# Kernel tuning notes

Hardware: AMD Instinct MI355X
Metric: run time of the kernel (lower is better)

## Reference

```python
import jax, jax.numpy as jnp
import numpy as np

D_MODEL = 1024
NUM_HEADS = 16
D_K = D_MODEL // NUM_HEADS
NEG_INF = -1e9


def setup_inputs() -> dict:
    key = jax.random.key(0)
    ks = jax.random.split(key, 12)
    B, S = 2, 2048
    Q = jax.random.normal(ks[0], (B, S, D_MODEL), jnp.float32)
    K = jax.random.normal(ks[1], (B, S, D_MODEL), jnp.float32)
    V = jax.random.normal(ks[2], (B, S, D_MODEL), jnp.float32)
    mask = jax.random.randint(ks[3], (B, 1, 1, S), 0, 2, jnp.int32)
    scale = 1.0 / np.sqrt(D_MODEL)
    WQ = jax.random.normal(ks[4], (D_MODEL, D_MODEL), jnp.float32) * scale
    bQ = jnp.zeros((D_MODEL,), jnp.float32)
    WK = jax.random.normal(ks[5], (D_MODEL, D_MODEL), jnp.float32) * scale
    bK = jnp.zeros((D_MODEL,), jnp.float32)
    WV = jax.random.normal(ks[6], (D_MODEL, D_MODEL), jnp.float32) * scale
    bV = jnp.zeros((D_MODEL,), jnp.float32)
    WO = jax.random.normal(ks[7], (D_MODEL, D_MODEL), jnp.float32) * scale
    bO = jnp.zeros((D_MODEL,), jnp.float32)
    return {"Q": Q, "K": K, "V": V, "mask": mask,
            "WQ": WQ, "bQ": bQ, "WK": WK, "bK": bK,
            "WV": WV, "bV": bV, "WO": WO, "bO": bO}


def _split_heads(x):
    # (B, S, d_model) -> (B, H, S, d_k)
    B, S, _ = x.shape
    return x.reshape(B, S, NUM_HEADS, D_K).transpose(0, 2, 1, 3)


def reference(Q, K, V, mask, WQ, bQ, WK, bK, WV, bV, WO, bO):
    B, Sq, _ = Q.shape
    q = _split_heads(Q @ WQ + bQ)   # (B, H, Sq, d_k)
    k = _split_heads(K @ WK + bK)   # (B, H, Sk, d_k)
    v = _split_heads(V @ WV + bV)   # (B, H, Sk, d_v)
    scores = jnp.einsum('bhqd,bhkd->bhqk', q, k) / jnp.sqrt(jnp.float32(D_K))
    scores = jnp.where(mask == 0, jnp.float32(NEG_INF), scores)
    attention = jax.nn.softmax(scores, axis=-1)         # (B, H, Sq, Sk)
    context = jnp.einsum('bhqk,bhkd->bhqd', attention, v)
    context = context.transpose(0, 2, 1, 3).reshape(B, Sq, D_MODEL)
    output = context @ WO + bO
    return (output, attention)
```

## Files before the change

### kernel.cpp

```cpp
#include <hip/hip_runtime.h>

typedef __attribute__((ext_vector_type(8))) __bf16 bf16x8;
typedef __attribute__((ext_vector_type(4))) __bf16 bf16x4;
typedef __attribute__((ext_vector_type(4))) float f32x4;

#define DEVFN static __device__ __forceinline__

#if __has_builtin(__builtin_amdgcn_exp2f)
#define EXP2(x) __builtin_amdgcn_exp2f(x)
#else
#define EXP2(x) exp2f(x)
#endif

DEVFN f32x4 mfma16(bf16x8 a, bf16x8 b, f32x4 c) {
  return __builtin_amdgcn_mfma_f32_16x16x32_bf16(a, b, c, 0, 0, 0);
}

DEVFN void gload16(const void* g, void* l) {
  __builtin_amdgcn_global_load_lds((const __attribute__((address_space(1))) void*)g,
                                   (__attribute__((address_space(3))) void*)l, 16, 0, 0);
}

__global__ __launch_bounds__(256) void transW4(const float* __restrict__ w0,
                                               const float* __restrict__ w1,
                                               const float* __restrict__ w2,
                                               const float* __restrict__ w3,
                                               unsigned short* __restrict__ obase) {
  __shared__ float t[64][65];
  const float* W = blockIdx.z == 0 ? w0 : blockIdx.z == 1 ? w1 : blockIdx.z == 2 ? w2 : w3;
  unsigned short* Wt = obase + ((size_t)blockIdx.z << 20);
  int k0 = blockIdx.x * 64, n0 = blockIdx.y * 64;
  int tid = threadIdx.x;
#pragma unroll
  for (int it = 0; it < 4; ++it) {
    int r = it * 16 + (tid >> 4);
    int c = (tid & 15) * 4;
    float4 v = *(const float4*)(W + (size_t)(k0 + r) * 1024 + n0 + c);
    t[r][c] = v.x; t[r][c + 1] = v.y; t[r][c + 2] = v.z; t[r][c + 3] = v.w;
  }
  __syncthreads();
#pragma unroll
  for (int it = 0; it < 2; ++it) {
    int nl = it * 32 + (tid >> 3);
    int kc = tid & 7;
    bf16x8 o;
#pragma unroll
    for (int j = 0; j < 8; ++j) o[j] = (__bf16)t[kc * 8 + j][nl];
    int n = n0 + nl;
    char* dst = (char*)Wt + (size_t)n * 2048 + (k0 << 1) + ((kc ^ (n & 7)) << 4);
    *(bf16x8*)dst = o;
  }
}

struct GArg {
  const void* A;
  const unsigned short* Bt;
  const float* bias;
  void* out;
  float scale;
};

template <int BM, int BN, int WR, int WC, int AF32, int EPI>
__global__ __launch_bounds__(256, 2) void gemm_t(GArg g0, GArg g1, GArg g2) {
  GArg g = blockIdx.z == 0 ? g0 : blockIdx.z == 1 ? g1 : g2;
  constexpr int MT = BM / WR / 16, NT = BN / WC / 16;
  constexpr int AB = AF32 ? 4 : 2;
  __shared__ char lA[BM * 64 * AB];
  __shared__ char lB[BN * 64 * 2];
  int tid = threadIdx.x, wave = tid >> 6, lane = tid & 63;
  int hi = lane >> 4, lo = lane & 15;
  int m0 = blockIdx.x * BM, n0 = blockIdx.y * BN;
  int wr = wave / WC, wc = wave % WC;
  f32x4 acc[MT][NT];
#pragma unroll
  for (int mt = 0; mt < MT; ++mt)
#pragma unroll
    for (int nt = 0; nt < NT; ++nt) acc[mt][nt] = (f32x4){0.f, 0.f, 0.f, 0.f};

  for (int k0 = 0; k0 < 1024; k0 += 64) {
    if (AF32) {
#pragma unroll
      for (int i = 0; i < BM / 16; ++i) {
        int off = i * 4096 + tid * 16;
        int row = off >> 8, b = off & 255;
        gload16((const char*)g.A + (size_t)(m0 + row) * 4096 + (k0 << 2)
                    + (b ^ ((row & 7) << 4)),
                lA + i * 4096 + wave * 1024);
      }
    } else {
#pragma unroll
      for (int i = 0; i < BM / 32; ++i) {
        int off = i * 4096 + tid * 16;
        int row = off >> 7, b = off & 127;
        gload16((const char*)g.A + (size_t)(m0 + row) * 2048 + (k0 << 1) + b,
                lA + i * 4096 + wave * 1024);
      }
    }
#pragma unroll
    for (int i = 0; i < BN / 32; ++i) {
      int off = i * 4096 + tid * 16;
      int row = off >> 7, b = off & 127;
      gload16((const char*)g.Bt + (size_t)(n0 + row) * 2048 + (k0 << 1) + b,
              lB + i * 4096 + wave * 1024);
    }
    __syncthreads();
#pragma unroll
    for (int kk = 0; kk < 2; ++kk) {
      bf16x8 af[MT], bfr[NT];
#pragma unroll
      for (int mt = 0; mt < MT; ++mt) {
        int row = wr * (BM / WR) + mt * 16 + lo;
        if (AF32) {
          int base = (row << 8) + ((kk << 7) + (hi << 5));
          int sw = (row & 7) << 4;
          f32x4 a0 = *(const f32x4*)(lA + ((base) ^ sw));
          f32x4 a1 = *(const f32x4*)(lA + ((base + 16) ^ sw));
          bf16x8 v;
#pragma unroll
          for (int j = 0; j < 4; ++j) { v[j] = (__bf16)a0[j]; v[4 + j] = (__bf16)a1[j]; }
          af[mt] = v;
        } else {
          int ob = (row << 7) + ((((kk << 2) + hi) << 4) ^ ((row & 7) << 4));
          af[mt] = *(const bf16x8*)(lA + ob);
        }
      }
#pragma unroll
      for (int nt = 0; nt < NT; ++nt) {
        int row = wc * (BN / WC) + nt * 16 + lo;
        int ob = (row << 7) + ((((kk << 2) + hi) << 4) ^ ((row & 7) << 4));
        bfr[nt] = *(const bf16x8*)(lB + ob);
      }
#pragma unroll
      for (int mt = 0; mt < MT; ++mt)
#pragma unroll
        for (int nt = 0; nt < NT; ++nt)
          acc[mt][nt] = mfma16(af[mt], bfr[nt], acc[mt][nt]);
    }
    __syncthreads();
  }

#pragma unroll
  for (int mt = 0; mt < MT; ++mt) {
#pragma unroll
    for (int nt = 0; nt < NT; ++nt) {
      int col = n0 + wc * (BN / WC) + nt * 16 + lo;
      float bs = g.bias[col];
      int row0 = m0 + wr * (BM / WR) + mt * 16 + (hi << 2);
      float vj[4];
#pragma unroll
      for (int j = 0; j < 4; ++j) vj[j] = (acc[mt][nt][j] + bs) * g.scale;
      if (EPI == 1) {
#pragma unroll
        for (int j = 0; j < 4; ++j)
          ((float*)g.out)[(size_t)(row0 + j) * 1024 + col] = vj[j];
      } else if (blockIdx.z == 2) {
        int d = col & 63;
        int bh = (row0 >> 11) * 16 + (col >> 6);
        int s = row0 & 2047;
        bf16x4 o;
#pragma unroll
        for (int j = 0; j < 4; ++j) o[j] = (__bf16)vj[j];
        char* p = (char*)g.out + ((size_t)bh << 18) + (size_t)d * 4096
                  + (s >> 6) * 128 + (((((s & 63) >> 3) ^ (d & 7)) << 4))
                  + ((s & 7) << 1);
        *(bf16x4*)p = o;
      } else {
#pragma unroll
        for (int j = 0; j < 4; ++j) {
          int srow = row0 + j;
          size_t hb = ((size_t)((srow >> 11) * 16 + (col >> 6))) << 18;
          int ib = ((srow & 2047) << 7) + (((col & 63) << 1) ^ ((srow & 7) << 4));
          *(__bf16*)((char*)g.out + hb + ib) = (__bf16)vj[j];
        }
      }
    }
  }
}

__global__ __launch_bounds__(256, 4) void attn_k(
    const unsigned short* __restrict__ qh, const unsigned short* __restrict__ kh,
    const unsigned short* __restrict__ vt, const int* __restrict__ mask,
    float* __restrict__ attn, unsigned short* __restrict__ ctx) {
  constexpr int S = 2048;
  __shared__ unsigned short ktl[64 * 64];
  __shared__ unsigned short vtl[64 * 64];
  __shared__ unsigned long long mkb[32];
  __shared__ float pf[4][16 * 68];

  int tid = threadIdx.x, wave = tid >> 6, lane = tid & 63;
  int hi = lane >> 4, lo = lane & 15;
  int f = blockIdx.y * 32 + blockIdx.x;
  int xcd = f & 7, slot = f >> 3;
  int bh = xcd * 4 + (slot & 3);
  int qb = slot >> 2;
  int b = bh >> 4, h = bh & 15;
  const char* khead = (const char*)kh + ((size_t)bh << 18);
  const char* qhead = (const char*)qh + ((size_t)bh << 18);
  const char* vhead = (const char*)vt + ((size_t)bh << 18);

  for (int it = 0; it < 8; ++it) {
    unsigned long long bal = __ballot(mask[b * S + it * 256 + tid] != 0);
    if (lane == 0) mkb[it * 4 + wave] = bal;
  }
  __syncthreads();

  int q0 = qb * 64 + wave * 16;
  bf16x8 qf[2];
  {
    int row = q0 + lo;
#pragma unroll
    for (int kk = 0; kk < 2; ++kk) {
      int ib = (row << 7) + ((((kk << 2) + hi) << 4) ^ ((row & 7) << 4));
      qf[kk] = *(const bf16x8*)(qhead + ib);
    }
  }

  float lsum[4] = {0.f, 0.f, 0.f, 0.f};

#pragma unroll
  for (int i = 0; i < 2; ++i)
    gload16(khead + i * 4096 + tid * 16, (char*)ktl + i * 4096 + wave * 1024);
  for (int kt = 0; kt < 32; ++kt) {
    const char* cb = (kt & 1) ? (const char*)vtl : (const char*)ktl;
    char* nb = (kt & 1) ? (char*)ktl : (char*)vtl;
    if (kt < 31) {
#pragma unroll
      for (int i = 0; i < 2; ++i)
        gload16(khead + (size_t)(kt + 1) * 8192 + i * 4096 + tid * 16,
                nb + i * 4096 + wave * 1024);
      asm volatile("s_waitcnt vmcnt(2)" ::: "memory");
    } else {
      asm volatile("s_waitcnt vmcnt(0)" ::: "memory");
    }
    __builtin_amdgcn_sched_barrier(0);
    __builtin_amdgcn_s_barrier();
    unsigned long long mw = mkb[kt];
    __builtin_amdgcn_s_setprio(1);
#pragma unroll
    for (int nt = 0; nt < 4; ++nt) {
      int r = nt * 16 + lo;
      f32x4 a = {0.f, 0.f, 0.f, 0.f};
#pragma unroll
      for (int kk = 0; kk < 2; ++kk) {
        int ob = (r << 7) + ((((kk << 2) + hi) << 4) ^ ((r & 7) << 4));
        a = mfma16(qf[kk], *(const bf16x8*)(cb + ob), a);
      }
      bool ok = (mw >> r) & 1ull;
#pragma unroll
      for (int j = 0; j < 4; ++j) lsum[j] += ok ? EXP2(a[j]) : 0.f;
    }
    __builtin_amdgcn_s_setprio(0);
    __builtin_amdgcn_s_barrier();
  }

  float rcp[4];
#pragma unroll
  for (int j = 0; j < 4; ++j) {
    float s = lsum[j];
    s += __shfl_xor(s, 1); s += __shfl_xor(s, 2);
    s += __shfl_xor(s, 4); s += __shfl_xor(s, 8);
    rcp[j] = s > 0.f ? 1.0f / s : 0.f;
  }

  f32x4 cacc[4];
#pragma unroll
  for (int nt = 0; nt < 4; ++nt) cacc[nt] = (f32x4){0.f, 0.f, 0.f, 0.f};

  float* arow = attn + (size_t)bh * S * S;
  float* pfw = pf[wave];

  for (int kt = 0; kt < 32; ++kt) {
#pragma unroll
    for (int i = 0; i < 2; ++i)
      gload16(khead + (size_t)kt * 8192 + i * 4096 + tid * 16,
              (char*)ktl + i * 4096 + wave * 1024);
#pragma unroll
    for (int i = 0; i < 2; ++i) {
      int off = i * 4096 + tid * 16;
      int d = off >> 7, x = off & 127;
      gload16(vhead + (size_t)d * 4096 + kt * 128 + x,
              (char*)vtl + i * 4096 + wave * 1024);
    }
    __syncthreads();
    unsigned long long mw = mkb[kt];
    __builtin_amdgcn_s_setprio(1);
#pragma unroll
    for (int nt = 0; nt < 4; ++nt) {
      int r = nt * 16 + lo;
      f32x4 a = {0.f, 0.f, 0.f, 0.f};
#pragma unroll
      for (int kk = 0; kk < 2; ++kk) {
        int ob = (r << 7) + ((((kk << 2) + hi) << 4) ^ ((r & 7) << 4));
        a = mfma16(qf[kk], *(const bf16x8*)((const char*)ktl + ob), a);
      }
      bool ok = (mw >> r) & 1ull;
#pragma unroll
      for (int j = 0; j < 4; ++j) {
        float pn = ok ? EXP2(a[j]) * rcp[j] : 0.f;
        pfw[((hi << 2) + j) * 68 + r] = pn;
      }
    }
#pragma unroll
    for (int c = 0; c < 2; ++c) {
      f32x4 p0 = *(const f32x4*)&pfw[lo * 68 + c * 32 + hi * 8];
      f32x4 p1 = *(const f32x4*)&pfw[lo * 68 + c * 32 + hi * 8 + 4];
      bf16x8 pa;
#pragma unroll
      for (int i = 0; i < 4; ++i) { pa[i] = (__bf16)p0[i]; pa[4 + i] = (__bf16)p1[i]; }
#pragma unroll
      for (int nt = 0; nt < 4; ++nt) {
        int d = nt * 16 + lo;
        int ob = (d << 7) + ((((c << 2) + hi) << 4) ^ ((d & 7) << 4));
        cacc[nt] = mfma16(pa, *(const bf16x8*)((const char*)vtl + ob), cacc[nt]);
      }
    }
    __builtin_amdgcn_s_setprio(0);
    {
      int rsub = lane >> 4;
      int cb = (lane & 15) << 2;
#pragma unroll
      for (int s = 0; s < 4; ++s) {
        int row = s * 4 + rsub;
        f32x4 v = *(const f32x4*)&pfw[row * 68 + cb];
        __builtin_nontemporal_store(
            v, (f32x4*)(arow + (size_t)(q0 + row) * S + kt * 64 + cb));
      }
    }
    __syncthreads();
  }

#pragma unroll
  for (int nt = 0; nt < 4; ++nt) {
#pragma unroll
    for (int j = 0; j < 4; ++j) {
      int s = q0 + (hi << 2) + j;
      int mrow = b * S + s;
      int n = h * 64 + nt * 16 + lo;
      int ib = (n << 1) ^ ((mrow & 7) << 4);
      *(__bf16*)((char*)ctx + (size_t)mrow * 2048 + ib) = (__bf16)cacc[nt][j];
    }
  }
}

extern "C" void kernel_launch(void* const* d_in, const int* in_sizes, int n_in,
                              void* d_out, int out_size, void* d_ws, size_t ws_size,
                              hipStream_t stream) {
  const float* Q  = (const float*)d_in[0];
  const float* K  = (const float*)d_in[1];
  const float* V  = (const float*)d_in[2];
  const int* mask = (const int*)d_in[3];
  const float* WQ = (const float*)d_in[4];
  const float* bQ = (const float*)d_in[5];
  const float* WK = (const float*)d_in[6];
  const float* bK = (const float*)d_in[7];
  const float* WV = (const float*)d_in[8];
  const float* bV = (const float*)d_in[9];
  const float* WO = (const float*)d_in[10];
  const float* bO = (const float*)d_in[11];

  char* ws = (char*)d_ws;
  const size_t M1 = 1ull << 20;
  unsigned short* WQt = (unsigned short*)(ws + 0 * M1);
  unsigned short* WKt = (unsigned short*)(ws + 2 * M1);
  unsigned short* WVt = (unsigned short*)(ws + 4 * M1);
  unsigned short* WOt = (unsigned short*)(ws + 6 * M1);
  unsigned short* qh  = (unsigned short*)(ws + 8 * M1);
  unsigned short* kh  = (unsigned short*)(ws + 16 * M1);
  unsigned short* vt  = (unsigned short*)(ws + 24 * M1);
  unsigned short* ctx = (unsigned short*)(ws + 32 * M1);

  float* outF = (float*)d_out;
  float* attn = (float*)d_out + 4194304;

  dim3 blk(256);
  const float qscale = 0.125f * 1.44269504088896340736f;

  transW4<<<dim3(16, 16, 4), blk, 0, stream>>>(WQ, WK, WV, WO, WQt);

  GArg aq{Q, WQt, bQ, qh, qscale};
  GArg ak{K, WKt, bK, kh, 1.f};
  GArg av{V, WVt, bV, vt, 1.f};
  gemm_t<128, 128, 2, 2, 1, 0><<<dim3(32, 8, 3), blk, 0, stream>>>(aq, ak, av);

  attn_k<<<dim3(32, 32), blk, 0, stream>>>(qh, kh, vt, mask, attn, ctx);

  GArg ao{ctx, WOt, bO, outF, 1.f};
  gemm_t<64, 128, 1, 4, 0, 1><<<dim3(64, 8, 1), blk, 0, stream>>>(ao, ao, ao);
}
```

Baseline: 246.4 us.

## Rework attention pass-1 K loading, reorder attention stores, raise QKV GEMM occupancy

The first (row-sum) pass of the attention kernel drops its double-buffered, prefetching K loop. It now loads two 64-key tiles into both LDS buffers at once, with a full __syncthreads, and processes them as one 128-key step. This halves the number of barriers but gives up the overlap between loads and compute. In the second pass the attention-probability store to global memory moves ahead of the P·V MFMAs and becomes a normal store instead of a nontemporal one. The QKV projection GEMM gets a launch-bounds occupancy hint of 3 blocks per CU instead of 2, which may limit its registers.

```diff
diff --git a/kernel.cpp b/kernel.cpp
--- a/kernel.cpp
+++ b/kernel.cpp
@@ -60,8 +60,8 @@
   float scale;
 };
 
-template <int BM, int BN, int WR, int WC, int AF32, int EPI>
-__global__ __launch_bounds__(256, 2) void gemm_t(GArg g0, GArg g1, GArg g2) {
+template <int BM, int BN, int WR, int WC, int AF32, int EPI, int OCC>
+__global__ __launch_bounds__(256, OCC) void gemm_t(GArg g0, GArg g1, GArg g2) {
   GArg g = blockIdx.z == 0 ? g0 : blockIdx.z == 1 ? g1 : g2;
   constexpr int MT = BM / WR / 16, NT = BN / WC / 16;
   constexpr int AB = AF32 ? 4 : 2;
@@ -217,40 +217,37 @@
 
   float lsum[4] = {0.f, 0.f, 0.f, 0.f};
 
-#pragma unroll
-  for (int i = 0; i < 2; ++i)
-    gload16(khead + i * 4096 + tid * 16, (char*)ktl + i * 4096 + wave * 1024);
-  for (int kt = 0; kt < 32; ++kt) {
-    const char* cb = (kt & 1) ? (const char*)vtl : (const char*)ktl;
-    char* nb = (kt & 1) ? (char*)ktl : (char*)vtl;
-    if (kt < 31) {
-#pragma unroll
-      for (int i = 0; i < 2; ++i)
-        gload16(khead + (size_t)(kt + 1) * 8192 + i * 4096 + tid * 16,
-                nb + i * 4096 + wave * 1024);
-      asm volatile("s_waitcnt vmcnt(2)" ::: "memory");
-    } else {
-      asm volatile("s_waitcnt vmcnt(0)" ::: "memory");
-    }
-    __builtin_amdgcn_sched_barrier(0);
-    __builtin_amdgcn_s_barrier();
-    unsigned long long mw = mkb[kt];
+  for (int kt2 = 0; kt2 < 16; ++kt2) {
+#pragma unroll
+    for (int i = 0; i < 2; ++i)
+      gload16(khead + (size_t)kt2 * 16384 + i * 4096 + tid * 16,
+              (char*)ktl + i * 4096 + wave * 1024);
+#pragma unroll
+    for (int i = 0; i < 2; ++i)
+      gload16(khead + (size_t)kt2 * 16384 + 8192 + i * 4096 + tid * 16,
+              (char*)vtl + i * 4096 + wave * 1024);
+    __syncthreads();
     __builtin_amdgcn_s_setprio(1);
 #pragma unroll
-    for (int nt = 0; nt < 4; ++nt) {
-      int r = nt * 16 + lo;
-      f32x4 a = {0.f, 0.f, 0.f, 0.f};
-#pragma unroll
-      for (int kk = 0; kk < 2; ++kk) {
-        int ob = (r << 7) + ((((kk << 2) + hi) << 4) ^ ((r & 7) << 4));
-        a = mfma16(qf[kk], *(const bf16x8*)(cb + ob), a);
-      }
-      bool ok = (mw >> r) & 1ull;
-#pragma unroll
-      for (int j = 0; j < 4; ++j) lsum[j] += ok ? EXP2(a[j]) : 0.f;
+    for (int half = 0; half < 2; ++half) {
+      unsigned long long mw = mkb[kt2 * 2 + half];
+      const char* buf = half ? (const char*)vtl : (const char*)ktl;
+#pragma unroll
+      for (int ntl = 0; ntl < 4; ++ntl) {
+        int r = ntl * 16 + lo;
+        f32x4 a = {0.f, 0.f, 0.f, 0.f};
+#pragma unroll
+        for (int kk = 0; kk < 2; ++kk) {
+          int ob = (r << 7) + ((((kk << 2) + hi) << 4) ^ ((r & 7) << 4));
+          a = mfma16(qf[kk], *(const bf16x8*)(buf + ob), a);
+        }
+        bool ok = (mw >> r) & 1ull;
+#pragma unroll
+        for (int j = 0; j < 4; ++j) lsum[j] += ok ? EXP2(a[j]) : 0.f;
+      }
     }
     __builtin_amdgcn_s_setprio(0);
-    __builtin_amdgcn_s_barrier();
+    __syncthreads();
   }
 
   float rcp[4];
@@ -300,6 +297,18 @@
         pfw[((hi << 2) + j) * 68 + r] = pn;
       }
     }
+    __builtin_amdgcn_s_setprio(0);
+    {
+      int rsub = lane >> 4;
+      int cb = (lane & 15) << 2;
+#pragma unroll
+      for (int s = 0; s < 4; ++s) {
+        int row = s * 4 + rsub;
+        f32x4 v = *(const f32x4*)&pfw[row * 68 + cb];
+        *(f32x4*)(arow + (size_t)(q0 + row) * S + kt * 64 + cb) = v;
+      }
+    }
+    __builtin_amdgcn_s_setprio(1);
 #pragma unroll
     for (int c = 0; c < 2; ++c) {
       f32x4 p0 = *(const f32x4*)&pfw[lo * 68 + c * 32 + hi * 8];
@@ -315,17 +324,6 @@
       }
     }
     __builtin_amdgcn_s_setprio(0);
-    {
-      int rsub = lane >> 4;
-      int cb = (lane & 15) << 2;
-#pragma unroll
-      for (int s = 0; s < 4; ++s) {
-        int row = s * 4 + rsub;
-        f32x4 v = *(const f32x4*)&pfw[row * 68 + cb];
-        __builtin_nontemporal_store(
-            v, (f32x4*)(arow + (size_t)(q0 + row) * S + kt * 64 + cb));
-      }
-    }
     __syncthreads();
   }
 
@@ -380,10 +378,10 @@
   GArg aq{Q, WQt, bQ, qh, qscale};
   GArg ak{K, WKt, bK, kh, 1.f};
   GArg av{V, WVt, bV, vt, 1.f};
-  gemm_t<128, 128, 2, 2, 1, 0><<<dim3(32, 8, 3), blk, 0, stream>>>(aq, ak, av);
+  gemm_t<128, 128, 2, 2, 1, 0, 3><<<dim3(32, 8, 3), blk, 0, stream>>>(aq, ak, av);
 
   attn_k<<<dim3(32, 32), blk, 0, stream>>>(qh, kh, vt, mask, attn, ctx);
 
   GArg ao{ctx, WOt, bO, outF, 1.f};
-  gemm_t<64, 128, 1, 4, 0, 1><<<dim3(64, 8, 1), blk, 0, stream>>>(ao, ao, ao);
-}
+  gemm_t<64, 128, 1, 4, 0, 1, 2><<<dim3(64, 8, 1), blk, 0, stream>>>(ao, ao, ao);
+}
```

After: 264.2 us. +7.2%, slower.
